# Performance work log

Hardware: AMD Instinct MI355X
Metric: run time of the kernel (lower is better)

The kernel has to match this reference:

```python
import jax, jax.numpy as jnp
import numpy as np

DIM = 96
NH = 8
HID = int(DIM * 2.66)  # 255
B, H, W = 2, 128, 128


def _conv(x, w, groups=1, pad=0):
    # NCHW conv, stride 1
    return jax.lax.conv_general_dilated(
        x, w, (1, 1), ((pad, pad), (pad, pad)),
        feature_group_count=groups,
        dimension_numbers=('NCHW', 'OIHW', 'NCHW'))


def _ln(x, w, b):
    # WithBias LayerNorm over the channel axis (torch does to_3d -> LN(dim) -> to_4d)
    mu = x.mean(axis=1, keepdims=True)
    var = ((x - mu) ** 2).mean(axis=1, keepdims=True)
    return (x - mu) * jax.lax.rsqrt(var + 1e-5) * w[None, :, None, None] + b[None, :, None, None]


def setup_inputs() -> dict:
    key = jax.random.key(0)
    ks = jax.random.split(key, 16)
    d, h2, h4 = DIM, 2 * HID, 4 * HID
    def n(k, shape, s):
        return jax.random.normal(k, shape, jnp.float32) * s
    return {
        'x': jax.random.normal(ks[0], (B, d, H, W), jnp.float32),
        'norm1_w': jnp.ones((d,), jnp.float32), 'norm1_b': jnp.zeros((d,), jnp.float32),
        'qkv_w': n(ks[1], (3 * d, d, 1, 1), 0.05),
        'qkv_dw_w': n(ks[2], (3 * d, 1, 3, 3), 0.1),
        'proj_w': n(ks[3], (d, d, 1, 1), 0.05),
        'temperature': jnp.ones((NH, 1, 1), jnp.float32),
        'thresholdweight': 0.2 * jnp.ones((4, 1, 1, 1), jnp.float32),
        'attn_w1': n(ks[4], (4, NH, NH), 0.2), 'attn_b1': jnp.zeros((4, NH), jnp.float32),
        'attn_w2': n(ks[5], (4, NH, NH), 0.2), 'attn_b2': jnp.zeros((4, NH), jnp.float32),
        'norm2_w': jnp.ones((d,), jnp.float32), 'norm2_b': jnp.zeros((d,), jnp.float32),
        'in_w': n(ks[6], (h2, d, 1, 1), 0.05),
        'main_w': n(ks[7], (h4, 1, 3, 3), 0.1),   # groups=2*HID, 2 out per group
        'lp_w': n(ks[8], (h4, 1, 3, 3), 0.1),     # depthwise
        'hp_w': n(ks[9], (h4, 1, 3, 3), 0.1),     # depthwise
        'ld_w': n(ks[10], (HID, 4, 3, 3), 0.1),   # groups=HID, 4 in per group
        'hd_w': n(ks[11], (HID, 4, 3, 3), 0.1),
        'out_w': n(ks[12], (d, h2, 1, 1), 0.05),
    }


def reference(x, norm1_w, norm1_b, qkv_w, qkv_dw_w, proj_w, temperature,
              thresholdweight, attn_w1, attn_b1, attn_w2, attn_b2,
              norm2_w, norm2_b, in_w, main_w, lp_w, hp_w, ld_w, hd_w, out_w):
    b, c, hh, ww = x.shape
    ch = c // NH
    # ---- STS channel attention ----
    xn = _ln(x, norm1_w, norm1_b)
    qkv = _conv(_conv(xn, qkv_w), qkv_dw_w, groups=3 * c, pad=1)
    q, k, v = jnp.split(qkv, 3, axis=1)
    q = q.reshape(b, NH, ch, hh * ww)
    k = k.reshape(b, NH, ch, hh * ww)
    v = v.reshape(b, NH, ch, hh * ww)
    q = q / jnp.maximum(jnp.linalg.norm(q, axis=-1, keepdims=True), 1e-12)
    k = k / jnp.maximum(jnp.linalg.norm(k, axis=-1, keepdims=True), 1e-12)
    attn = jnp.einsum('bhcn,bhdn->bhcd', q, k) * temperature[None]  # [b,NH,ch,ch]

    def sts_gen(w1, b1, w2, b2):
        a_abs = jnp.abs(attn)
        avg = a_abs.mean(axis=(-2, -1))                       # [b, NH] (GAP)
        g = jax.nn.sigmoid(jnp.maximum(avg @ w1.T + b1, 0.0) @ w2.T + b2)
        thr = (avg * g)[:, :, None, None]
        return jnp.sign(attn) * jnp.maximum(a_abs - thr, 0.0)

    comp = jax.vmap(sts_gen)(attn_w1, attn_b1, attn_w2, attn_b2)  # [4,b,NH,ch,ch]
    comp = jax.nn.softmax(comp, axis=-1)
    attn_c = jnp.sum(comp * thresholdweight.reshape(4, 1, 1, 1, 1), axis=0)
    out = jnp.einsum('bhcd,bhdn->bhcn', attn_c, v).reshape(b, c, hh, ww)
    x = x + _conv(out, proj_w)

    # ---- DeCoupleConvv3 FFN ----
    y = _ln(x, norm2_w, norm2_b)
    y = _conv(y, in_w)                                         # [b, 2*HID, h, w]
    y = jax.nn.relu(_conv(y, main_w, groups=2 * HID, pad=1))   # [b, 4*HID, h, w]
    avg_w = jnp.full((4 * HID, 1, 3, 3), 1.0 / 9.0, y.dtype)   # fixed, non-trainable
    yp = jnp.pad(y, ((0, 0), (0, 0), (1, 1), (1, 1)), mode='edge')  # replicate pad
    l = _conv(yp, avg_w, groups=4 * HID, pad=0)
    hb = y - l
    l = jax.nn.relu(_conv(l, lp_w, groups=4 * HID, pad=1))
    hb = jax.nn.relu(_conv(hb, hp_w, groups=4 * HID, pad=1))
    l_tol, l_toh = jnp.split(l, [2 * HID], axis=1)
    h_toh, h_tol = jnp.split(hb, [2 * HID], axis=1)
    l2 = jax.nn.relu(_conv(jnp.concatenate([l_tol, h_tol], axis=1), ld_w, groups=HID, pad=1))
    h2 = jax.nn.relu(_conv(jnp.concatenate([h_toh, l_toh], axis=1), hd_w, groups=HID, pad=1))
    ffo = _conv(jnp.concatenate([l2, h2], axis=1), out_w)
    return x + ffo
```

## Files before the change

kernel.cpp:

```cpp
#include <hip/hip_runtime.h>
#include <hip/hip_bf16.h>
#include <hip/hip_fp16.h>

#define NB   2
#define NC   96
#define NW   128
#define NPIX 16384
#define NHD  8
#define CHD  12
#define HIDC 255
#define H2C  510
#define H4C  1020

typedef __hip_bfloat16 bf16;
typedef unsigned short u16;
typedef unsigned int   u32;
typedef __half2 h2t;

typedef __attribute__((ext_vector_type(8))) __bf16 bfrag;
typedef __attribute__((ext_vector_type(4))) float  ffrag;

__device__ __forceinline__ float bfu(u16 u)  { return __uint_as_float(((u32)u) << 16); }
__device__ __forceinline__ float bflo(u32 u) { return __uint_as_float(u << 16); }
__device__ __forceinline__ float bfhi(u32 u) { return __uint_as_float(u & 0xffff0000u); }
__device__ __forceinline__ u16 f2u16(float a) {
    bf16 x = __float2bfloat16(a); return *(u16*)&x;
}
__device__ __forceinline__ u32 packbf(float a, float b) {
    return (u32)f2u16(a) | ((u32)f2u16(b) << 16);
}
__device__ __forceinline__ uint4 pack8(const float o[8]) {
    uint4 r; r.x = packbf(o[0], o[1]); r.y = packbf(o[2], o[3]);
    r.z = packbf(o[4], o[5]); r.w = packbf(o[6], o[7]); return r;
}

__device__ __forceinline__ h2t H2u(u32 v) { return __builtin_bit_cast(h2t, v); }
__device__ __forceinline__ u32 U32h(h2t v) { return __builtin_bit_cast(u32, v); }
__device__ __forceinline__ h2t relu2(h2t v) {
    u32 r, u = U32h(v);
    asm("v_pk_max_f16 %0, %1, 0" : "=v"(r) : "v"(u));
    return H2u(r);
}
__device__ __forceinline__ h2t wtap(const h2t* a, int idx) {
    u32 u = U32h(a[idx >> 1]);
    u32 r = (idx & 1) ? ((u & 0xFFFF0000u) | (u >> 16)) : ((u << 16) | (u & 0xFFFFu));
    return H2u(r);
}

struct Trip { h2t L, C, R; };
__device__ __forceinline__ Trip shift3(h2t c2, bool repl, int lane) {
    u32 d = U32h(c2);
    u32 up = (u32)__shfl_up((int)d, 1);
    u32 dn = (u32)__shfl_down((int)d, 1);
    if (lane == 0)  up = repl ? (d << 16) : 0u;
    if (lane == 63) dn = repl ? (d >> 16) : 0u;
    Trip t; t.C = c2;
    t.L = H2u((up >> 16) | (d << 16));
    t.R = H2u((d >> 16) | (dn << 16));
    return t;
}
__device__ __forceinline__ h2t ldrow2(const u16* base, int row, int lane) {
    return ((unsigned)row < 128u) ? *(const h2t*)(base + row * NW + lane * 2) : H2u(0u);
}
#define CONV3(W, c, T, Pa, Pb, Pc)                                             \
    Pc = __hfma2(wtap(W, (c)*9+0), T.L, __hfma2(wtap(W, (c)*9+1), T.C,         \
         __hfma2(wtap(W, (c)*9+2), T.R, Pc)));                                 \
    Pb = __hfma2(wtap(W, (c)*9+3), T.L, __hfma2(wtap(W, (c)*9+4), T.C,         \
         __hfma2(wtap(W, (c)*9+5), T.R, Pb)));                                 \
    Pa = __hfma2(wtap(W, (c)*9+6), T.L, __hfma2(wtap(W, (c)*9+7), T.C,         \
         __hfma2(wtap(W, (c)*9+8), T.R, Pa)));

__global__ __launch_bounds__(64) void ffnstream_kernel(
    const u16* __restrict__ yi, const float* __restrict__ main_w,
    const float* __restrict__ lp_w, const float* __restrict__ hp_w,
    const float* __restrict__ ld_w, const float* __restrict__ hd_w,
    u16* __restrict__ cat) {
    const int lane = threadIdx.x;
    const int g = blockIdx.y;
    const int R0 = blockIdx.x * 32, R1 = R0 + 32;
    const int L0 = max(R0 - 2, 0), L1 = min(R1 + 1, 127);
    const int P0 = max(R0 - 1, 0), P1 = min(R1, 127);
    const u16* yib = yi + (size_t)blockIdx.z * H2C * NPIX;
    u16* catb = cat + (size_t)blockIdx.z * H2C * NPIX;
    const u16* s0p = yib + (size_t)(2 * g) * NPIX;
    const u16* s1p = yib + (size_t)(2 * g + 1) * NPIX;

    h2t wm[18], wl[18], wh[18], wd[18], we[18];
    {
        const float* pm = main_w + 36 * g;
        const float* pl = lp_w + 36 * g;
        const float* ph = hp_w + 36 * g;
        const float* pd = ld_w + 36 * g;
        const float* pe = hd_w + 36 * g;
        #pragma unroll
        for (int k = 0; k < 18; ++k) {
            wm[k] = __halves2half2(__float2half(pm[2*k]), __float2half(pm[2*k+1]));
            wl[k] = __halves2half2(__float2half(pl[2*k]), __float2half(pl[2*k+1]));
            wh[k] = __halves2half2(__float2half(ph[2*k]), __float2half(ph[2*k+1]));
            wd[k] = __halves2half2(__float2half(pd[2*k]), __float2half(pd[2*k+1]));
            we[k] = __halves2half2(__float2half(pe[2*k]), __float2half(pe[2*k+1]));
        }
    }
    const h2t z = H2u(0u);
    const __half k9h = __float2half(1.f / 9.f);
    const h2t k9 = __halves2half2(k9h, k9h);

    h2t ymP0[4], ymP1[4], ymP2[4];
    h2t ymRa[4], ymRb[4], ymRc[4];
    h2t lpP0[4], lpP1[4], lpP2[4];
    h2t hpP0[4], hpP1[4], hpP2[4];
    h2t cd0 = z, cd1 = z, cd2 = z;
    h2t ce0 = z, ce1 = z, ce2 = z;
    #pragma unroll
    for (int c = 0; c < 4; ++c) {
        ymP0[c] = ymP1[c] = ymP2[c] = z;
        ymRa[c] = ymRb[c] = ymRc[c] = z;
        lpP0[c] = lpP1[c] = lpP2[c] = z;
        hpP0[c] = hpP1[c] = hpP2[c] = z;
    }

    const int ys = max(R0 - 3, 0) - 1;
    const int ye = R1 + 3;
    h2t cur0 = ldrow2(s0p, ys, lane),     cur1 = ldrow2(s1p, ys, lane);
    h2t nx10 = ldrow2(s0p, ys + 1, lane), nx11 = ldrow2(s1p, ys + 1, lane);
    #pragma unroll 3
    for (int yy = ys; yy <= ye; ++yy) {
        h2t nx20 = ldrow2(s0p, yy + 2, lane), nx21 = ldrow2(s1p, yy + 2, lane);
        {
            Trip t0 = shift3(cur0, false, lane);
            Trip t1 = shift3(cur1, false, lane);
            CONV3(wm, 0, t0, ymP0[0], ymP1[0], ymP2[0]);
            CONV3(wm, 1, t0, ymP0[1], ymP1[1], ymP2[1]);
            CONV3(wm, 2, t1, ymP0[2], ymP1[2], ymP2[2]);
            CONV3(wm, 3, t1, ymP0[3], ymP1[3], ymP2[3]);
        }
        #pragma unroll
        for (int c = 0; c < 4; ++c) {
            h2t n = relu2(ymP0[c]);
            ymRc[c] = ymRb[c]; ymRb[c] = ymRa[c]; ymRa[c] = n;
            ymP0[c] = ymP1[c]; ymP1[c] = ymP2[c]; ymP2[c] = z;
        }
        int y_l = yy - 2;
        if (y_l >= L0 && y_l <= L1) {
            #pragma unroll
            for (int c = 0; c < 4; ++c) {
                h2t top = (y_l == 0)   ? ymRb[c] : ymRc[c];
                h2t bot = (y_l == 127) ? ymRb[c] : ymRa[c];
                h2t vs = __hadd2(__hadd2(top, ymRb[c]), bot);
                Trip tv = shift3(vs, true, lane);
                h2t l  = __hmul2(__hadd2(__hadd2(tv.L, tv.C), tv.R), k9);
                h2t hb = __hsub2(ymRb[c], l);
                Trip tl = shift3(l, false, lane);
                CONV3(wl, c, tl, lpP0[c], lpP1[c], lpP2[c]);
                Trip th = shift3(hb, false, lane);
                CONV3(wh, c, th, hpP0[c], hpP1[c], hpP2[c]);
            }
        }
        int y_p = yy - 3;
        {
            h2t lpN[4], hpN[4];
            #pragma unroll
            for (int c = 0; c < 4; ++c) {
                lpN[c] = relu2(lpP0[c]); hpN[c] = relu2(hpP0[c]);
                lpP0[c] = lpP1[c]; lpP1[c] = lpP2[c]; lpP2[c] = z;
                hpP0[c] = hpP1[c]; hpP1[c] = hpP2[c]; hpP2[c] = z;
            }
            if (y_p >= P0 && y_p <= P1) {
                #pragma unroll
                for (int c = 0; c < 4; ++c) {
                    bool low = (4 * g + c) < H2C;
                    h2t sld = low ? lpN[c] : hpN[c];
                    h2t shd = low ? hpN[c] : lpN[c];
                    Trip ts = shift3(sld, false, lane);
                    CONV3(wd, c, ts, cd0, cd1, cd2);
                    Trip tu = shift3(shd, false, lane);
                    CONV3(we, c, tu, ce0, ce1, ce2);
                }
            }
        }
        int y_c = yy - 4;
        if (y_c >= R0 && y_c < R1) {
            float a0 = fmaxf(__low2float(cd0), 0.f), a1 = fmaxf(__high2float(cd0), 0.f);
            float b0 = fmaxf(__low2float(ce0), 0.f), b1 = fmaxf(__high2float(ce0), 0.f);
            *(u32*)(catb + (size_t)g * NPIX + y_c * NW + lane * 2) = packbf(a0, a1);
            *(u32*)(catb + (size_t)(HIDC + g) * NPIX + y_c * NW + lane * 2) = packbf(b0, b1);
        }
        cd0 = cd1; cd1 = cd2; cd2 = z;
        ce0 = ce1; ce1 = ce2; ce2 = z;
        cur0 = nx10; cur1 = nx11;
        nx10 = nx20; nx11 = nx21;
    }
}

template <typename TOut, bool RES, int OFMT, bool LNF = false, int MT = 64>
__global__ __launch_bounds__(256) void gemm1x1_kernel(
    const u16* __restrict__ Bm, const float* __restrict__ Am,
    const float* __restrict__ res, TOut* __restrict__ Cm,
    int M, int K, size_t strideB, size_t strideC, size_t strideA,
    const float* __restrict__ xf, const float* __restrict__ lng,
    const float* __restrict__ lnb) {
    __shared__ u16 Ash[MT * 40];
    __shared__ u16 Bsh[128 * 40];
    __shared__ float lmu[128], linv[128];
    __shared__ float sred[2][128], qred[2][128];
    const u16* Bz = Bm + (size_t)blockIdx.z * strideB;
    const float* Az = Am + (size_t)blockIdx.z * strideA;
    const float* xz = LNF ? (xf + (size_t)blockIdx.z * NC * NPIX) : nullptr;
    int n0 = blockIdx.x * 128;
    int m0 = blockIdx.y * MT;
    int tid = threadIdx.x;
    int w = tid >> 6, l15 = tid & 15, q = (tid & 63) >> 4;
    int amm = tid >> 2, akc = (tid & 3) * 8;
    int bkk = tid >> 3, bs0 = tid & 7;

    if constexpr (LNF) {
        int p = tid & 127, hh = tid >> 7;
        float s = 0.f, s2 = 0.f;
        #pragma unroll
        for (int c = 0; c < 48; ++c) {
            float v = xz[(size_t)(hh * 48 + c) * NPIX + n0 + p];
            s += v; s2 += v * v;
        }
        sred[hh][p] = s; qred[hh][p] = s2;
        __syncthreads();
        if (tid < 128) {
            float S = sred[0][tid] + sred[1][tid];
            float Q = qred[0][tid] + qred[1][tid];
            float m = S * (1.f / NC);
            float va = Q * (1.f / NC) - m * m;
            lmu[tid] = m; linv[tid] = rsqrtf(va + 1e-5f);
        }
        __syncthreads();
    }

    constexpr int NH = MT / 64;
    ffrag acc[NH][8];
    #pragma unroll
    for (int mt = 0; mt < NH; ++mt)
        #pragma unroll
        for (int nt = 0; nt < 8; ++nt)
            #pragma unroll
            for (int e = 0; e < 4; ++e) acc[mt][nt][e] = 0.f;

    for (int k0 = 0; k0 < K; k0 += 32) {
        #pragma unroll
        for (int half = 0; half < NH; ++half) {
            int gm = m0 + half * 64 + amm;
            float f[8];
            #pragma unroll
            for (int e = 0; e < 8; ++e) {
                int gk = k0 + akc + e;
                f[e] = (gm < M && gk < K) ? Az[(size_t)gm * K + gk] : 0.f;
            }
            u32* dst = (u32*)&Ash[(half * 64 + amm) * 40 + akc];
            #pragma unroll
            for (int e = 0; e < 4; ++e) dst[e] = packbf(f[2 * e], f[2 * e + 1]);
        }
        if constexpr (LNF) {
            int gk = k0 + bkk;
            const float* src = xz + (size_t)gk * NPIX + n0;
            float gc = lng[gk], bc = lnb[gk];
            #pragma unroll
            for (int pass = 0; pass < 2; ++pass) {
                int nn = (bs0 + pass * 8) * 8;
                float4 f0 = *(const float4*)(src + nn);
                float4 f1 = *(const float4*)(src + nn + 4);
                float f[8] = {f0.x, f0.y, f0.z, f0.w, f1.x, f1.y, f1.z, f1.w};
                #pragma unroll
                for (int e = 0; e < 8; ++e) {
                    float nv = (f[e] - lmu[nn + e]) * linv[nn + e] * gc + bc;
                    Bsh[(nn + e) * 40 + bkk] = f2u16(nv);
                }
            }
        } else {
            int gk = k0 + bkk;
            bool ok = gk < K;
            const u16* src = Bz + (size_t)gk * NPIX + n0;
            #pragma unroll
            for (int pass = 0; pass < 2; ++pass) {
                int nn = (bs0 + pass * 8) * 8;
                if (ok) {
                    uint4 v = *(const uint4*)(src + nn);
                    Bsh[(nn + 0) * 40 + bkk] = (u16)(v.x & 0xffff);
                    Bsh[(nn + 1) * 40 + bkk] = (u16)(v.x >> 16);
                    Bsh[(nn + 2) * 40 + bkk] = (u16)(v.y & 0xffff);
                    Bsh[(nn + 3) * 40 + bkk] = (u16)(v.y >> 16);
                    Bsh[(nn + 4) * 40 + bkk] = (u16)(v.z & 0xffff);
                    Bsh[(nn + 5) * 40 + bkk] = (u16)(v.z >> 16);
                    Bsh[(nn + 6) * 40 + bkk] = (u16)(v.w & 0xffff);
                    Bsh[(nn + 7) * 40 + bkk] = (u16)(v.w >> 16);
                } else {
                    #pragma unroll
                    for (int e = 0; e < 8; ++e) Bsh[(nn + e) * 40 + bkk] = 0;
                }
            }
        }
        __syncthreads();
        bfrag af[NH];
        #pragma unroll
        for (int half = 0; half < NH; ++half)
            af[half] = *(const bfrag*)&Ash[(half * 64 + w * 16 + l15) * 40 + q * 8];
        #pragma unroll
        for (int nt = 0; nt < 8; ++nt) {
            bfrag bf = *(const bfrag*)&Bsh[(nt * 16 + l15) * 40 + q * 8];
            #pragma unroll
            for (int half = 0; half < NH; ++half)
                acc[half][nt] = __builtin_amdgcn_mfma_f32_16x16x32_bf16(af[half], bf, acc[half][nt], 0, 0, 0);
        }
        __syncthreads();
    }
    TOut* Cz = Cm + (size_t)blockIdx.z * strideC;
    const float* rz = res + (RES ? (size_t)blockIdx.z * strideC : 0);
    #pragma unroll
    for (int mt = 0; mt < NH; ++mt) {
        int mrow = m0 + mt * 64 + w * 16 + q * 4;
        #pragma unroll
        for (int nt = 0; nt < 8; ++nt) {
            int col = n0 + nt * 16 + l15;
            #pragma unroll
            for (int r = 0; r < 4; ++r) {
                int row = mrow + r;
                if (row < M) {
                    float v = acc[mt][nt][r];
                    if (RES) v += rz[(size_t)row * NPIX + col];
                    if constexpr (OFMT == 0) {
                        ((float*)Cz)[(size_t)row * NPIX + col] = v;
                    } else if constexpr (OFMT == 1) {
                        ((u16*)Cz)[(size_t)row * NPIX + col] = f2u16(v);
                    } else {
                        __half hh = __float2half(v);
                        ((u16*)Cz)[(size_t)row * NPIX + col] = __builtin_bit_cast(u16, hh);
                    }
                }
            }
        }
    }
}

__device__ __forceinline__ void load_row_zpad(const u16* ib, int iy, int x0, float a[10]) {
    if (iy < 0 || iy >= NW) {
        #pragma unroll
        for (int k = 0; k < 10; ++k) a[k] = 0.f;
        return;
    }
    const u16* rp = ib + iy * NW;
    uint4 v = *(const uint4*)(rp + x0);
    a[1]=bflo(v.x); a[2]=bfhi(v.x); a[3]=bflo(v.y); a[4]=bfhi(v.y);
    a[5]=bflo(v.z); a[6]=bfhi(v.z); a[7]=bflo(v.w); a[8]=bfhi(v.w);
    a[0] = (x0 > 0)   ? bfu(rp[x0 - 1]) : 0.f;
    a[9] = (x0 < 120) ? bfu(rp[x0 + 8]) : 0.f;
}

template <bool RELU>
__global__ __launch_bounds__(256) void dwconv3x3_kernel(
    const u16* __restrict__ in, const float* __restrict__ w,
    u16* __restrict__ out, int CHN, int ICN, int idiv,
    float* __restrict__ sqsum) {
    int id = blockIdx.x * 256 + threadIdx.x;
    int ty = id >> 4, tx = id & 15;
    int y0 = ty * 4, x0 = tx * 8;
    int b = blockIdx.y / CHN, oc = blockIdx.y % CHN;
    int ic = oc / idiv;
    const u16* ib = in + ((size_t)b * ICN + ic) * NPIX;
    float a[6][10];
    #pragma unroll
    for (int k = 0; k < 6; ++k) load_row_zpad(ib, y0 - 1 + k, x0, a[k]);
    const float* wr = w + (size_t)oc * 9;
    float w9[9];
    #pragma unroll
    for (int k = 0; k < 9; ++k) w9[k] = wr[k];
    u16* ob = out + ((size_t)b * CHN + oc) * NPIX + y0 * NW + x0;
    float s2 = 0.f;
    #pragma unroll
    for (int jr = 0; jr < 4; ++jr) {
        float o[8];
        #pragma unroll
        for (int j = 0; j < 8; ++j) {
            float s = 0.f;
            #pragma unroll
            for (int r = 0; r < 3; ++r)
                #pragma unroll
                for (int kx = 0; kx < 3; ++kx)
                    s += w9[r * 3 + kx] * a[jr + r][j + kx];
            o[j] = RELU ? fmaxf(s, 0.f) : s;
            s2 += o[j] * o[j];
        }
        *(uint4*)(ob + jr * NW) = pack8(o);
    }
    if (oc < 192) {
        #pragma unroll
        for (int off = 32; off > 0; off >>= 1) s2 += __shfl_down(s2, off, 64);
        __shared__ float prt[4];
        int wid = threadIdx.x >> 6;
        if ((threadIdx.x & 63) == 0) prt[wid] = s2;
        __syncthreads();
        if (threadIdx.x == 0)
            atomicAdd(&sqsum[b * 192 + oc], prt[0] + prt[1] + prt[2] + prt[3]);
    }
}

__global__ __launch_bounds__(256) void attn_kernel(
    const u16* __restrict__ qkv2, float* __restrict__ attn_raw) {
    int blk = blockIdx.y;
    int slice = blockIdx.x;
    int i = blk % CHD; int h = (blk / CHD) % NHD; int b = blk / (CHD * NHD);
    const u16* q = qkv2 + ((size_t)b * 288 + h * CHD + i) * NPIX;
    const u16* k = qkv2 + ((size_t)b * 288 + 96 + h * CHD) * NPIX;
    float acc[CHD];
    #pragma unroll
    for (int j = 0; j < CHD; ++j) acc[j] = 0.f;
    int p0 = slice * 4096;
    #pragma unroll
    for (int it = 0; it < 2; ++it) {
        int p = p0 + it * 2048 + threadIdx.x * 8;
        uint4 qv = *(const uint4*)(q + p);
        float qf[8];
        qf[0]=bflo(qv.x); qf[1]=bfhi(qv.x); qf[2]=bflo(qv.y); qf[3]=bfhi(qv.y);
        qf[4]=bflo(qv.z); qf[5]=bfhi(qv.z); qf[6]=bflo(qv.w); qf[7]=bfhi(qv.w);
        #pragma unroll
        for (int j = 0; j < CHD; ++j) {
            uint4 kv = *(const uint4*)(k + (size_t)j * NPIX + p);
            float s = qf[0]*bflo(kv.x) + qf[1]*bfhi(kv.x) + qf[2]*bflo(kv.y) + qf[3]*bfhi(kv.y)
                    + qf[4]*bflo(kv.z) + qf[5]*bfhi(kv.z) + qf[6]*bflo(kv.w) + qf[7]*bfhi(kv.w);
            acc[j] += s;
        }
    }
    __shared__ float part[4][CHD];
    int wid = threadIdx.x >> 6, lane = threadIdx.x & 63;
    #pragma unroll
    for (int j = 0; j < CHD; ++j) {
        float v = acc[j];
        #pragma unroll
        for (int off = 32; off > 0; off >>= 1) v += __shfl_down(v, off, 64);
        if (lane == 0) part[wid][j] = v;
    }
    __syncthreads();
    if (threadIdx.x < CHD) {
        int j = threadIdx.x;
        float d = part[0][j] + part[1][j] + part[2][j] + part[3][j];
        atomicAdd(&attn_raw[(size_t)blk * CHD + j], d);
    }
}

__global__ __launch_bounds__(256) void sts_kernel(
    const float* __restrict__ attn, const float* __restrict__ sclr,
    const float* __restrict__ temp, const float* __restrict__ tw,
    const float* __restrict__ w1, const float* __restrict__ b1,
    const float* __restrict__ w2, const float* __restrict__ b2,
    const float* __restrict__ proj_w, float* __restrict__ Wm) {
    int b = blockIdx.x;
    __shared__ float sat[NHD * CHD * CHD];
    __shared__ float sac[NHD * CHD * CHD];
    __shared__ float srs[192];
    __shared__ float pavg[NHD * CHD];
    __shared__ float avg[NHD];
    __shared__ float thr[4][NHD];
    if (threadIdx.x < 192) {
        float r = sclr[b * 192 + threadIdx.x];
        srs[threadIdx.x] = 1.f / fmaxf(sqrtf(r), 1e-12f);
    }
    __syncthreads();
    for (int idx = threadIdx.x; idx < NHD * CHD * CHD; idx += 256) {
        int h = idx / (CHD * CHD); int r = idx % (CHD * CHD);
        int i = r / CHD, j = r % CHD;
        sat[idx] = attn[(size_t)b * NHD * CHD * CHD + idx]
                 * srs[h * CHD + i] * srs[96 + h * CHD + j] * temp[h];
    }
    __syncthreads();
    if (threadIdx.x < NHD * CHD) {
        float s = 0.f;
        const float* row = sat + threadIdx.x * CHD;
        #pragma unroll
        for (int j = 0; j < CHD; ++j) s += fabsf(row[j]);
        pavg[threadIdx.x] = s;
    }
    __syncthreads();
    if (threadIdx.x < NHD) {
        float s = 0.f;
        #pragma unroll
        for (int i = 0; i < CHD; ++i) s += pavg[threadIdx.x * CHD + i];
        avg[threadIdx.x] = s * (1.f / (CHD * CHD));
    }
    __syncthreads();
    if (threadIdx.x < 4) {
        int s = threadIdx.x;
        float t1[NHD];
        for (int hp = 0; hp < NHD; ++hp) {
            float u = b1[s * NHD + hp];
            for (int h = 0; h < NHD; ++h) u += avg[h] * w1[s * 64 + hp * NHD + h];
            t1[hp] = fmaxf(u, 0.f);
        }
        for (int hp = 0; hp < NHD; ++hp) {
            float u = b2[s * NHD + hp];
            for (int h = 0; h < NHD; ++h) u += t1[h] * w2[s * 64 + hp * NHD + h];
            float gg = 1.f / (1.f + expf(-u));
            thr[s][hp] = avg[hp] * gg;
        }
    }
    __syncthreads();
    if (threadIdx.x < NHD * CHD) {
        int h = threadIdx.x / CHD, i = threadIdx.x % CHD;
        const float* arow = sat + (h * CHD + i) * CHD;
        float acc[CHD];
        #pragma unroll
        for (int j = 0; j < CHD; ++j) acc[j] = 0.f;
        for (int s = 0; s < 4; ++s) {
            float comp[CHD]; float m = -1e30f;
            #pragma unroll
            for (int j = 0; j < CHD; ++j) {
                float a = arow[j];
                float sg = (a > 0.f) ? 1.f : ((a < 0.f) ? -1.f : 0.f);
                float c = sg * fmaxf(fabsf(a) - thr[s][h], 0.f);
                comp[j] = c; m = fmaxf(m, c);
            }
            float sum = 0.f;
            #pragma unroll
            for (int j = 0; j < CHD; ++j) { comp[j] = expf(comp[j] - m); sum += comp[j]; }
            float wts2v = tw[s] / sum;
            #pragma unroll
            for (int j = 0; j < CHD; ++j) acc[j] += wts2v * comp[j];
        }
        for (int j = 0; j < CHD; ++j)
            sac[(h * CHD + i) * CHD + j] = acc[j];
    }
    __syncthreads();
    float* Wb = Wm + (size_t)b * NC * NC;
    for (int idx = threadIdx.x; idx < NC * NC; idx += 256) {
        int m = idx / NC, col = idx % NC;
        int h = col / CHD, j = col % CHD;
        const float* pr = proj_w + m * NC + h * CHD;
        const float* ar = sac + h * CHD * CHD + j;
        float s = 0.f;
        #pragma unroll
        for (int i = 0; i < CHD; ++i) s += pr[i] * ar[i * CHD];
        Wb[idx] = s;
    }
}

extern "C" void kernel_launch(void* const* d_in, const int* in_sizes, int n_in,
                              void* d_out, int out_size, void* d_ws, size_t ws_size,
                              hipStream_t stream) {
    const float* x       = (const float*)d_in[0];
    const float* norm1_w = (const float*)d_in[1];
    const float* norm1_b = (const float*)d_in[2];
    const float* qkv_w   = (const float*)d_in[3];
    const float* qkv_dw  = (const float*)d_in[4];
    const float* proj_w  = (const float*)d_in[5];
    const float* temp    = (const float*)d_in[6];
    const float* thw     = (const float*)d_in[7];
    const float* aw1     = (const float*)d_in[8];
    const float* ab1     = (const float*)d_in[9];
    const float* aw2     = (const float*)d_in[10];
    const float* ab2     = (const float*)d_in[11];
    const float* norm2_w = (const float*)d_in[12];
    const float* norm2_b = (const float*)d_in[13];
    const float* in_w    = (const float*)d_in[14];
    const float* main_w  = (const float*)d_in[15];
    const float* lp_w    = (const float*)d_in[16];
    const float* hp_w    = (const float*)d_in[17];
    const float* ld_w    = (const float*)d_in[18];
    const float* hd_w    = (const float*)d_in[19];
    const float* out_w   = (const float*)d_in[20];
    float* out = (float*)d_out;

    char* ws = (char*)d_ws;
    float* x1    = (float*)(ws + 0);
    u16*   qkv1  = (u16*)(ws + 18874368);
    u16*   qkv2  = (u16*)(ws + 37748736);
    float* scl   = (float*)(ws + 56623104);
    float* attn  = (float*)(ws + 56624640);
    char*  F0    = ws + 56672256;
    float* Wm    = (float*)(ws + 56655872);
    const size_t S_full = 33423360;
    bool full = ws_size >= (size_t)56672256 + S_full;

    dim3 blk(256);
    (void)hipMemsetAsync(scl, 0, 10752, stream);
    gemm1x1_kernel<u16, false, 1, true, 128><<<dim3(128, 3, NB), blk, 0, stream>>>(
        nullptr, qkv_w, nullptr, qkv1, 288, 96, 0, (size_t)288 * NPIX, 0,
        x, norm1_w, norm1_b);
    dwconv3x3_kernel<false><<<dim3(2, NB * 288), blk, 0, stream>>>(
        qkv1, qkv_dw, qkv2, 288, 288, 1, scl);
    attn_kernel<<<dim3(4, NB * NHD * CHD), blk, 0, stream>>>(qkv2, attn);
    sts_kernel<<<dim3(NB), blk, 0, stream>>>(attn, scl, temp, thw, aw1, ab1, aw2, ab2,
                                             proj_w, Wm);
    gemm1x1_kernel<float, true, 0, false, 64><<<dim3(128, 2, NB), blk, 0, stream>>>(
        qkv2 + (size_t)192 * NPIX, Wm, x, x1, 96, 96,
        (size_t)288 * NPIX, (size_t)NC * NPIX, (size_t)NC * NC,
        nullptr, nullptr, nullptr);
    if (full) {
        u16* yi  = qkv1;
        u16* cat = (u16*)F0;
        gemm1x1_kernel<u16, false, 2, true, 128><<<dim3(128, 4, NB), blk, 0, stream>>>(
            nullptr, in_w, nullptr, yi, H2C, 96, 0, (size_t)H2C * NPIX, 0,
            x1, norm2_w, norm2_b);
        ffnstream_kernel<<<dim3(4, HIDC, NB), dim3(64), 0, stream>>>(
            yi, main_w, lp_w, hp_w, ld_w, hd_w, cat);
        gemm1x1_kernel<float, true, 0, false, 64><<<dim3(128, 2, NB), blk, 0, stream>>>(
            cat, out_w, x1, out, 96, H2C, (size_t)H2C * NPIX, (size_t)NC * NPIX, 0,
            nullptr, nullptr, nullptr);
    } else {
        for (int b = 0; b < NB; ++b) {
            u16* yi  = qkv1;
            u16* cat = qkv2;
            gemm1x1_kernel<u16, false, 2, true, 128><<<dim3(128, 4, 1), blk, 0, stream>>>(
                nullptr, in_w, nullptr, yi, H2C, 96, 0, 0, 0,
                x1 + (size_t)b * NC * NPIX, norm2_w, norm2_b);
            ffnstream_kernel<<<dim3(4, HIDC, 1), dim3(64), 0, stream>>>(
                yi, main_w, lp_w, hp_w, ld_w, hd_w, cat);
            gemm1x1_kernel<float, true, 0, false, 64><<<dim3(128, 2, 1), blk, 0, stream>>>(
                cat, out_w, x1 + (size_t)b * NC * NPIX, out + (size_t)b * NC * NPIX,
                96, H2C, 0, 0, 0, nullptr, nullptr, nullptr);
        }
    }
}
```

Baseline: 353.5 us.

## Compute per-head QK^T attention scores with bf16 MFMA instead of scalar dots

The attention-score kernel now launches one block per (batch, head, pixel slice) instead of one per query row. Each wave computes the full 12x12 Q·K^T tile with 16x16x32 bf16 MFMA instructions, padding the channel dimension to 16, and the partial tiles are reduced through shared memory before an atomic add. This removes the 12-fold re-reading of K rows and the scalar FMA and shuffle-reduction work. In exchange, each block reads four extra channels beyond the head, and those products are computed and then discarded.

```diff
diff --git a/kernel.cpp b/kernel.cpp
--- a/kernel.cpp
+++ b/kernel.cpp
@@ -401,44 +401,33 @@
 
 __global__ __launch_bounds__(256) void attn_kernel(
     const u16* __restrict__ qkv2, float* __restrict__ attn_raw) {
-    int blk = blockIdx.y;
-    int slice = blockIdx.x;
-    int i = blk % CHD; int h = (blk / CHD) % NHD; int b = blk / (CHD * NHD);
-    const u16* q = qkv2 + ((size_t)b * 288 + h * CHD + i) * NPIX;
-    const u16* k = qkv2 + ((size_t)b * 288 + 96 + h * CHD) * NPIX;
-    float acc[CHD];
-    #pragma unroll
-    for (int j = 0; j < CHD; ++j) acc[j] = 0.f;
-    int p0 = slice * 4096;
-    #pragma unroll
-    for (int it = 0; it < 2; ++it) {
-        int p = p0 + it * 2048 + threadIdx.x * 8;
-        uint4 qv = *(const uint4*)(q + p);
-        float qf[8];
-        qf[0]=bflo(qv.x); qf[1]=bfhi(qv.x); qf[2]=bflo(qv.y); qf[3]=bfhi(qv.y);
-        qf[4]=bflo(qv.z); qf[5]=bfhi(qv.z); qf[6]=bflo(qv.w); qf[7]=bfhi(qv.w);
-        #pragma unroll
-        for (int j = 0; j < CHD; ++j) {
-            uint4 kv = *(const uint4*)(k + (size_t)j * NPIX + p);
-            float s = qf[0]*bflo(kv.x) + qf[1]*bfhi(kv.x) + qf[2]*bflo(kv.y) + qf[3]*bfhi(kv.y)
-                    + qf[4]*bflo(kv.z) + qf[5]*bfhi(kv.z) + qf[6]*bflo(kv.w) + qf[7]*bfhi(kv.w);
-            acc[j] += s;
-        }
-    }
-    __shared__ float part[4][CHD];
-    int wid = threadIdx.x >> 6, lane = threadIdx.x & 63;
-    #pragma unroll
-    for (int j = 0; j < CHD; ++j) {
-        float v = acc[j];
-        #pragma unroll
-        for (int off = 32; off > 0; off >>= 1) v += __shfl_down(v, off, 64);
-        if (lane == 0) part[wid][j] = v;
-    }
+    int wq = threadIdx.x >> 6, lane = threadIdx.x & 63;
+    int bh = blockIdx.y;
+    int b = bh / NHD, h = bh % NHD;
+    const u16* qb = qkv2 + ((size_t)b * 288 + h * CHD) * NPIX;
+    const u16* kb = qkv2 + ((size_t)b * 288 + 96 + h * CHD) * NPIX;
+    int ch = lane & 15;
+    int pxw = (blockIdx.x * 4 + wq) * 256 + ((lane >> 4) * 8);
+    ffrag acc;
+    #pragma unroll
+    for (int e = 0; e < 4; ++e) acc[e] = 0.f;
+    #pragma unroll
+    for (int c = 0; c < 8; ++c) {
+        int px = pxw + c * 32;
+        bfrag aq = *(const bfrag*)(qb + (size_t)ch * NPIX + px);
+        bfrag bk = *(const bfrag*)(kb + (size_t)ch * NPIX + px);
+        acc = __builtin_amdgcn_mfma_f32_16x16x32_bf16(aq, bk, acc, 0, 0, 0);
+    }
+    __shared__ float red[4][64][4];
+    #pragma unroll
+    for (int r = 0; r < 4; ++r) red[wq][lane][r] = acc[r];
     __syncthreads();
-    if (threadIdx.x < CHD) {
-        int j = threadIdx.x;
-        float d = part[0][j] + part[1][j] + part[2][j] + part[3][j];
-        atomicAdd(&attn_raw[(size_t)blk * CHD + j], d);
+    if (threadIdx.x < CHD * CHD) {
+        int i = threadIdx.x / CHD, j = threadIdx.x % CHD;
+        int l = ((i >> 2) << 4) | j;
+        int r = i & 3;
+        float s = red[0][l][r] + red[1][l][r] + red[2][l][r] + red[3][l][r];
+        atomicAdd(&attn_raw[((size_t)bh * CHD + i) * CHD + j], s);
     }
 }
 
@@ -581,7 +570,7 @@
         x, norm1_w, norm1_b);
     dwconv3x3_kernel<false><<<dim3(2, NB * 288), blk, 0, stream>>>(
         qkv1, qkv_dw, qkv2, 288, 288, 1, scl);
-    attn_kernel<<<dim3(4, NB * NHD * CHD), blk, 0, stream>>>(qkv2, attn);
+    attn_kernel<<<dim3(16, NB * NHD), blk, 0, stream>>>(qkv2, attn);
     sts_kernel<<<dim3(NB), blk, 0, stream>>>(attn, scl, temp, thw, aw1, ab1, aw2, ab2,
                                              proj_w, Wm);
     gemm1x1_kernel<float, true, 0, false, 64><<<dim3(128, 2, NB), blk, 0, stream>>>(
```

Result: no change. 349.7 us (median of 2 runs) (-1.1%).
